# Kernel tuning notes

Hardware: AMD Instinct MI355X
Metric: run time of the kernel (lower is better)

Reference implementation:

```python
import math
import jax, jax.numpy as jnp
import numpy as np

B, S, HID, H = 2, 1024, 2048, 16
D = HID // H
HEAVY_RATIO = 0.1
RECENT_RATIO = 0.1
ROPE_BASE = 10000.0
N_KEEP_DIMS = 6  # eviction zeroes all but the 6 largest-|k| dims


def setup_inputs() -> dict:
    key = jax.random.key(0)
    k1, k2, k3, k4, k5 = jax.random.split(key, 5)
    std = 0.02
    hidden_states = jax.random.normal(k1, (B, S, HID), jnp.float32)
    wq = jax.random.normal(k2, (HID, HID), jnp.float32) * std
    wk = jax.random.normal(k3, (HID, HID), jnp.float32) * std
    wv = jax.random.normal(k4, (HID, HID), jnp.float32) * std
    wo = jax.random.normal(k5, (HID, HID), jnp.float32) * std
    neg = jnp.finfo(jnp.float32).min
    causal = jnp.tril(jnp.ones((S, S), bool))
    attention_mask = jnp.broadcast_to(
        jnp.where(causal, 0.0, neg)[None, None], (B, 1, S, S)
    ).astype(jnp.float32)
    return {"hidden_states": hidden_states, "wq": wq, "wk": wk, "wv": wv,
            "wo": wo, "attention_mask": attention_mask}


def _rotate_half(x):
    return jnp.concatenate([-x[..., D // 2:], x[..., :D // 2]], axis=-1)


def _apply_rope(q, k):
    inv_freq = 1.0 / (ROPE_BASE ** (jnp.arange(0, D, 2, dtype=jnp.float32) / D))
    t = jnp.arange(S, dtype=jnp.float32)
    freqs = jnp.outer(t, inv_freq)              # [S, D/2]
    emb = jnp.concatenate([freqs, freqs], -1)   # [S, D]
    cos = jnp.cos(emb)[None, None]              # [1,1,S,D]
    sin = jnp.sin(emb)[None, None]
    return q * cos + _rotate_half(q) * sin, k * cos + _rotate_half(k) * sin


def _h2o_attention(q, k, heavy_budget, recent_budget):
    """Faithful vectorized form of low_dimension_attention.

    The torch loop mutates key_states in place by zeroing the (D-6)
    smallest-magnitude dims of one evicted token per step. Since the
    small-dim set is fixed per (b,h) and zeroing is idempotent, we carry a
    boolean evicted mask instead of the mutated key tensor.
    """
    cache_budget = heavy_budget + recent_budget
    scale = 1.0 / math.sqrt(D)
    # small_dimensions: computed once at first trigger (t = cache_budget+1)
    # from the first cache_budget (unmutated) keys.
    mean_abs = jnp.abs(k[:, :, :cache_budget, :]).mean(axis=2)      # [B,H,D]
    ranks = jnp.argsort(jnp.argsort(mean_abs, axis=-1), axis=-1)
    small_mask = ranks < (D - N_KEEP_DIMS)                          # [B,H,D]
    sidx = jnp.arange(S)

    def step(carry, xs):
        hist, evicted, prev_attn = carry
        t, q_t = xs                                                 # q_t: [B,H,D]
        pred = t > cache_budget
        limit = t - recent_budget if recent_budget > 0 else t
        # eviction score = inf-mask history + previous step's raw scores
        scores = jnp.where(sidx < limit, hist + prev_attn, jnp.inf)  # [B,H,S]
        idx = jnp.argmin(scores, axis=-1)                            # [B,H]
        do = pred & (sidx[None, None, :] == idx[..., None])          # [B,H,S]
        evicted = evicted | do
        hist = jnp.where(do, jnp.inf, hist)
        k_eff = jnp.where(evicted[..., None] & small_mask[:, :, None, :], 0.0, k)
        attn = jnp.einsum('bhd,bhsd->bhs', q_t, k_eff) * scale
        attn = jnp.where(sidx <= t, attn, 0.0)
        return (hist, evicted, attn), attn

    init = (jnp.zeros((B, H, S), jnp.float32),
            jnp.zeros((B, H, S), bool),
            jnp.zeros((B, H, S), jnp.float32))
    q_seq = jnp.moveaxis(q, 2, 0)                                    # [S,B,H,D]
    _, rows = jax.lax.scan(step, init, (jnp.arange(S), q_seq))       # [S,B,H,S]
    return jnp.moveaxis(rows, 0, 2)                                  # [B,H,S,S]


def reference(hidden_states, wq, wk, wv, wo, attention_mask):
    heavy_budget = int(HEAVY_RATIO * S)
    recent_budget = int(RECENT_RATIO * S)
    q = (hidden_states @ wq).reshape(B, S, H, D).transpose(0, 2, 1, 3)
    k = (hidden_states @ wk).reshape(B, S, H, D).transpose(0, 2, 1, 3)
    v = (hidden_states @ wv).reshape(B, S, H, D).transpose(0, 2, 1, 3)
    q, k = _apply_rope(q, k)
    attn_weights = _h2o_attention(q, k, heavy_budget, recent_budget)  # [B,H,S,S]
    attn_weights = jnp.maximum(attn_weights + attention_mask,
                               jnp.finfo(jnp.float32).min)
    attn_weights = jax.nn.softmax(attn_weights, axis=-1)
    out = jnp.einsum('bhqk,bhkd->bhqd', attn_weights, v)
    out = out.transpose(0, 2, 1, 3).reshape(B, S, HID)
    return out @ wo
```

## Files before the change

### kernel.cpp

```cpp
#include <hip/hip_runtime.h>
#include <math.h>

#define S_LEN    1024
#define NHEAD    16
#define DHEAD    128
#define HIDDEN   2048
#define BATCH    2
#define BH       32
#define CACHE_B  204
#define RECENT_B 102
#define QK_SCALE 0.08838834764831845f

typedef float v2f __attribute__((ext_vector_type(2)));
typedef float f32x4 __attribute__((ext_vector_type(4)));
typedef short short8v __attribute__((ext_vector_type(8)));

__device__ __forceinline__ unsigned short f2bf(float f) {
  unsigned u = __float_as_uint(f);
  u += 0x7fffu + ((u >> 16) & 1u);
  return (unsigned short)(u >> 16);
}
__device__ __forceinline__ float bf2f(unsigned short h) {
  return __uint_as_float(((unsigned)h) << 16);
}

__device__ __forceinline__ void gl16(const void* g, void* l) {
  __builtin_amdgcn_global_load_lds(
      (const __attribute__((address_space(1))) unsigned int*)g,
      (__attribute__((address_space(3))) unsigned int*)l, 16, 0, 0);
}

__device__ __forceinline__ void mfma_b(f32x4& d, short8v a, short8v b) {
  asm("v_mfma_f32_16x16x32_bf16 %0, %1, %2, %0" : "+v"(d) : "v"(a), "v"(b));
}

__global__ __launch_bounds__(256) void split_a(
    const float* __restrict__ X, unsigned short* __restrict__ hi,
    unsigned short* __restrict__ lo) {
  const size_t i = ((size_t)blockIdx.x * 256 + threadIdx.x) * 4;
  const float4 v = *(const float4*)&X[i];
  const float f[4] = {v.x, v.y, v.z, v.w};
  unsigned short h[4], l[4];
#pragma unroll
  for (int j = 0; j < 4; ++j) {
    h[j] = f2bf(f[j]);
    l[j] = f2bf(f[j] - bf2f(h[j]));
  }
  *(ushort4*)&hi[i] = make_ushort4(h[0], h[1], h[2], h[3]);
  *(ushort4*)&lo[i] = make_ushort4(l[0], l[1], l[2], l[3]);
}

__global__ __launch_bounds__(256) void split_T(
    const float* __restrict__ W0, const float* __restrict__ W1,
    const float* __restrict__ W2, unsigned short* __restrict__ outB) {
  __shared__ float Ts[64][65];
  const float* W = (blockIdx.z == 0) ? W0 : ((blockIdx.z == 1) ? W1 : W2);
  unsigned short* hiT = outB + (size_t)blockIdx.z * 8388608u;
  unsigned short* loT = hiT + 4194304u;
  const int k0 = blockIdx.y * 64, n0 = blockIdx.x * 64;
  const int r = threadIdx.x >> 4, c4 = (threadIdx.x & 15) * 4;
#pragma unroll
  for (int it = 0; it < 4; ++it) {
    const float4 v =
        *(const float4*)&W[(size_t)(k0 + it * 16 + r) * HIDDEN + n0 + c4];
    Ts[it * 16 + r][c4 + 0] = v.x;
    Ts[it * 16 + r][c4 + 1] = v.y;
    Ts[it * 16 + r][c4 + 2] = v.z;
    Ts[it * 16 + r][c4 + 3] = v.w;
  }
  __syncthreads();
#pragma unroll
  for (int it = 0; it < 4; ++it) {
    const int n = it * 16 + r;
    unsigned short h[4], l[4];
#pragma unroll
    for (int j = 0; j < 4; ++j) {
      const float f = Ts[c4 + j][n];
      h[j] = f2bf(f);
      l[j] = f2bf(f - bf2f(h[j]));
    }
    const size_t o = (size_t)(n0 + n) * HIDDEN + k0 + c4;
    *(ushort4*)&hiT[o] = make_ushort4(h[0], h[1], h[2], h[3]);
    *(ushort4*)&loT[o] = make_ushort4(l[0], l[1], l[2], l[3]);
  }
}

template <int MODE>
__global__ __launch_bounds__(256) void gemm_mfma(
    const unsigned short* __restrict__ Ahi,
    const unsigned short* __restrict__ Alo,
    const unsigned short* __restrict__ WT, float* __restrict__ C0) {
  __shared__ unsigned short AhS[128][32];
  __shared__ unsigned short AlS[128][32];
  __shared__ unsigned short BhS[128][32];
  __shared__ unsigned short BlS[128][32];
  const int tid = threadIdx.x;
  const int lane = tid & 63;
  const int wv = tid >> 6;
  const int wr = wv >> 1, wc = wv & 1;
  const int m0 = blockIdx.y * 128, n0 = blockIdx.x * 128;
  const unsigned short* BhiT =
      WT + (MODE == 0 ? (size_t)blockIdx.z * 8388608u : (size_t)0);
  const unsigned short* BloT = BhiT + 4194304u;

  f32x4 acc[4][4];
#pragma unroll
  for (int i = 0; i < 4; ++i)
#pragma unroll
    for (int j = 0; j < 4; ++j) acc[i][j] = (f32x4)(0.0f);

  const int r_st = tid >> 2;
  const int kc_st = (tid & 3) * 8;

  for (int k0 = 0; k0 < HIDDEN; k0 += 32) {
#pragma unroll
    for (int l = 0; l < 2; ++l) {
      const int r = r_st + l * 64;
      const size_t ga = (size_t)(m0 + r) * HIDDEN + (k0 + kc_st);
      const size_t gb = (size_t)(n0 + r) * HIDDEN + (k0 + kc_st);
      gl16(Ahi + ga, &AhS[r][kc_st]);
      gl16(Alo + ga, &AlS[r][kc_st]);
      gl16(BhiT + gb, &BhS[r][kc_st]);
      gl16(BloT + gb, &BlS[r][kc_st]);
    }
    __syncthreads();
    const int mrow = lane & 15;
    const int kb = (lane >> 4) * 8;
    short8v ah[4], al[4], bh[4], bl[4];
#pragma unroll
    for (int i = 0; i < 4; ++i) {
      ah[i] = *(const short8v*)&AhS[wr * 64 + i * 16 + mrow][kb];
      al[i] = *(const short8v*)&AlS[wr * 64 + i * 16 + mrow][kb];
      bh[i] = *(const short8v*)&BhS[wc * 64 + i * 16 + mrow][kb];
      bl[i] = *(const short8v*)&BlS[wc * 64 + i * 16 + mrow][kb];
    }
#pragma unroll
    for (int i = 0; i < 4; ++i)
#pragma unroll
      for (int j = 0; j < 4; ++j) {
        mfma_b(acc[i][j], ah[i], bh[j]);
        mfma_b(acc[i][j], al[i], bh[j]);
        mfma_b(acc[i][j], ah[i], bl[j]);
      }
    __syncthreads();
  }

  float* C = C0;
  if (MODE == 0) C += (size_t)blockIdx.z * ((size_t)BH * S_LEN * DHEAD);
#pragma unroll
  for (int i = 0; i < 4; ++i) {
    const int mbase = m0 + wr * 64 + i * 16 + ((lane >> 4) * 4);
#pragma unroll
    for (int j = 0; j < 4; ++j) {
      const int n = n0 + wc * 64 + j * 16 + (lane & 15);
#pragma unroll
      for (int rg = 0; rg < 4; ++rg) {
        const int m = mbase + rg;
        const float val = acc[i][j][rg];
        if (MODE == 0) {
          const int b = m >> 10, s = m & (S_LEN - 1);
          const int h = n >> 7, d = n & (DHEAD - 1);
          C[(((size_t)(b * NHEAD + h) * S_LEN + s) * DHEAD) + d] = val;
        } else {
          C[(size_t)m * HIDDEN + n] = val;
        }
      }
    }
  }
}

__global__ __launch_bounds__(256) void rope_qk(float* __restrict__ Q,
                                               float* __restrict__ K) {
  int g = blockIdx.x * 4 + (threadIdx.x >> 6);
  int lane = threadIdx.x & 63;
  int s = g & (S_LEN - 1);
  double invf = exp(-((double)(2 * lane) / 128.0) * log(10000.0));
  float angle = (float)s * (float)invf;
  float c = (float)cos((double)angle);
  float sn = (float)sin((double)angle);
  size_t base = (size_t)g * DHEAD;
  float q0 = Q[base + lane], q1 = Q[base + lane + 64];
  Q[base + lane] = q0 * c - q1 * sn;
  Q[base + lane + 64] = q1 * c + q0 * sn;
  float k0 = K[base + lane], k1 = K[base + lane + 64];
  K[base + lane] = k0 * c - k1 * sn;
  K[base + lane + 64] = k1 * c + k0 * sn;
}

__global__ __launch_bounds__(128) void keep_pack(
    const float* __restrict__ Q, const float* __restrict__ K,
    float* __restrict__ Qp, float* __restrict__ Kp) {
  int bh = blockIdx.x;
  int d = threadIdx.x;
  __shared__ float ma[128];
  __shared__ int kf[128];
  __shared__ int kidx[8];
  const float* Kb = K + (size_t)bh * S_LEN * DHEAD;
  const float* Qb = Q + (size_t)bh * S_LEN * DHEAD;
  float sum = 0.0f;
  for (int s = 0; s < CACHE_B; ++s) sum += fabsf(Kb[(size_t)s * DHEAD + d]);
  ma[d] = sum / 204.0f;
  __syncthreads();
  float v = ma[d];
  int rank = 0;
  for (int e = 0; e < 128; ++e) {
    float u = ma[e];
    rank += (u < v) || (u == v && e < d);
  }
  int keep = (rank >= 128 - 6);
  kf[d] = keep;
  __syncthreads();
  if (keep) {
    int pos = 0;
    for (int e = 0; e < d; ++e) pos += kf[e];
    kidx[pos] = d;
  }
  __syncthreads();
  int i0 = kidx[0], i1 = kidx[1], i2 = kidx[2];
  int i3 = kidx[3], i4 = kidx[4], i5 = kidx[5];
  for (int s = threadIdx.x; s < S_LEN; s += 128) {
    size_t src = (size_t)s * DHEAD;
    size_t dst = ((size_t)bh * S_LEN + s) * 8;
    Qp[dst + 0] = Qb[src + i0]; Qp[dst + 1] = Qb[src + i1];
    Qp[dst + 2] = Qb[src + i2]; Qp[dst + 3] = Qb[src + i3];
    Qp[dst + 4] = Qb[src + i4]; Qp[dst + 5] = Qb[src + i5];
    Kp[dst + 0] = Kb[src + i0]; Kp[dst + 1] = Kb[src + i1];
    Kp[dst + 2] = Kb[src + i2]; Kp[dst + 3] = Kb[src + i3];
    Kp[dst + 4] = Kb[src + i4]; Kp[dst + 5] = Kb[src + i5];
  }
}

__global__ __launch_bounds__(256) void qkt_scores(
    const float* __restrict__ Q, const float* __restrict__ K,
    float* __restrict__ Af) {
  if (blockIdx.x > blockIdx.y) return;
  __shared__ float Qs[16][132];
  __shared__ float Ks[16][132];
  const int bh = blockIdx.z;
  const int tid = threadIdx.x;
  const int tx = tid & 15, ty = tid >> 4;
  const int m0 = blockIdx.y * 128, n0 = blockIdx.x * 128;
  const float* Qb = Q + (size_t)bh * S_LEN * DHEAD;
  const float* Kb = K + (size_t)bh * S_LEN * DHEAD;
  v2f acc[8][4];
#pragma unroll
  for (int i = 0; i < 8; ++i)
#pragma unroll
    for (int p = 0; p < 4; ++p) acc[i][p] = (v2f)(0.0f);

  for (int k0 = 0; k0 < DHEAD; k0 += 16) {
#pragma unroll
    for (int l = 0; l < 2; ++l) {
      int f = tid + l * 256;
      int r = f >> 2, c = (f & 3) * 4;
      const float4 q = *(const float4*)&Qb[(size_t)(m0 + r) * DHEAD + k0 + c];
      Qs[c + 0][r] = q.x; Qs[c + 1][r] = q.y;
      Qs[c + 2][r] = q.z; Qs[c + 3][r] = q.w;
      const float4 kv = *(const float4*)&Kb[(size_t)(n0 + r) * DHEAD + k0 + c];
      Ks[c + 0][r] = kv.x; Ks[c + 1][r] = kv.y;
      Ks[c + 2][r] = kv.z; Ks[c + 3][r] = kv.w;
    }
    __syncthreads();
#pragma unroll
    for (int kk = 0; kk < 16; ++kk) {
      float av[8];
      v2f bv[4];
      *(float4*)&av[0] = *(float4*)&Qs[kk][ty * 4];
      *(float4*)&av[4] = *(float4*)&Qs[kk][64 + ty * 4];
      const float4 b0 = *(const float4*)&Ks[kk][tx * 4];
      const float4 b1 = *(const float4*)&Ks[kk][64 + tx * 4];
      bv[0] = (v2f){b0.x, b0.y};
      bv[1] = (v2f){b0.z, b0.w};
      bv[2] = (v2f){b1.x, b1.y};
      bv[3] = (v2f){b1.z, b1.w};
#pragma unroll
      for (int i = 0; i < 8; ++i) {
        const v2f a2 = (v2f){av[i], av[i]};
#pragma unroll
        for (int p = 0; p < 4; ++p) acc[i][p] = a2 * bv[p] + acc[i][p];
      }
    }
    __syncthreads();
  }
  float* Cb = Af + (size_t)bh * S_LEN * S_LEN;
#pragma unroll
  for (int gi = 0; gi < 2; ++gi)
#pragma unroll
    for (int i = 0; i < 4; ++i) {
      const int t = m0 + gi * 64 + ty * 4 + i;
      const int ia = gi * 4 + i;
#pragma unroll
      for (int gj = 0; gj < 2; ++gj) {
        const int s = n0 + gj * 64 + tx * 4;
        float4 o;
        o.x = acc[ia][gj * 2 + 0].x * QK_SCALE;
        o.y = acc[ia][gj * 2 + 0].y * QK_SCALE;
        o.z = acc[ia][gj * 2 + 1].x * QK_SCALE;
        o.w = acc[ia][gj * 2 + 1].y * QK_SCALE;
        *(float4*)&Cb[(size_t)t * S_LEN + s] = o;
      }
    }
}

template <int CTRL, int RMASK>
__device__ __forceinline__ float dpp_fmin(float x) {
  const int xi = __builtin_bit_cast(int, x);
  const int y = __builtin_amdgcn_update_dpp(xi, xi, CTRL, RMASK, 0xF, false);
  return fminf(x, __builtin_bit_cast(float, y));
}
__device__ __forceinline__ float wave_min_f32(float x) {
  x = dpp_fmin<0x111, 0xF>(x);
  x = dpp_fmin<0x112, 0xF>(x);
  x = dpp_fmin<0x114, 0xF>(x);
  x = dpp_fmin<0x118, 0xF>(x);
  x = dpp_fmin<0x142, 0xA>(x);
  x = dpp_fmin<0x143, 0xC>(x);
  return __builtin_bit_cast(
      float, __builtin_amdgcn_readlane(__builtin_bit_cast(int, x), 63));
}

__global__ __launch_bounds__(64, 1) void scan_evict(
    const float* __restrict__ Af, int* __restrict__ evt) {
  __shared__ int evt_lds[S_LEN];
  const int bh = blockIdx.x;
  const int lane = threadIdx.x;
  const float* Ab = Af + (size_t)bh * S_LEN * S_LEN;
  int* evtb = evt + bh * S_LEN;

  {
    const int4 big = make_int4(0x7fffffff, 0x7fffffff, 0x7fffffff, 0x7fffffff);
#pragma unroll
    for (int j = 0; j < 4; ++j) *(int4*)&evt_lds[j * 256 + lane * 4] = big;
  }

  unsigned evmask = 0;
  unsigned elig = (lane < 6) ? 0xFFFFu : (lane == 6 ? 0x7Fu : 0u);

  const float* lb = Ab + lane * 16;
  float4 A0[4], A1[4], A2[4], A3[4], A4[4], A5[4];

#define SB() __builtin_amdgcn_sched_barrier(0)

#define LDROW(R, r)                                      \
  do {                                                   \
    int r_ = (r);                                        \
    r_ = r_ > 1022 ? 1022 : r_;                          \
    const float* rb = lb + (size_t)r_ * S_LEN;           \
    R[0] = *(const float4*)(rb + 0);                     \
    R[1] = *(const float4*)(rb + 4);                     \
    R[2] = *(const float4*)(rb + 8);                     \
    R[3] = *(const float4*)(rb + 12);                    \
  } while (0)

#define STEP(R, T)                                                          \
  do {                                                                      \
    const int t_ = (T);                                                     \
    const int snew = t_ - 103;      \
    elig |= ((snew >> 4) == lane) ? (1u << (snew & 15)) : 0u;               \
    const unsigned ue = elig & ~evmask;                                     \
    float fv[16];                                                           \
    _Pragma("unroll") for (int p = 0; p < 4; ++p) {                         \
      fv[p * 4 + 0] = ((ue >> (p * 4 + 0)) & 1u) ? R[p].x : INFINITY;       \
      fv[p * 4 + 1] = ((ue >> (p * 4 + 1)) & 1u) ? R[p].y : INFINITY;       \
      fv[p * 4 + 2] = ((ue >> (p * 4 + 2)) & 1u) ? R[p].z : INFINITY;       \
      fv[p * 4 + 3] = ((ue >> (p * 4 + 3)) & 1u) ? R[p].w : INFINITY;       \
    }                                                                       \
            \
    float m8[8]; int s8[8];                                                 \
    _Pragma("unroll") for (int i = 0; i < 8; ++i) {                         \
      m8[i] = fminf(fv[2 * i], fv[2 * i + 1]);                              \
      s8[i] = (fv[2 * i] <= fv[2 * i + 1]) ? (2 * i) : (2 * i + 1);         \
    }                                                                       \
    float m4[4]; int s4[4];                                                 \
    _Pragma("unroll") for (int i = 0; i < 4; ++i) {                         \
      m4[i] = fminf(m8[2 * i], m8[2 * i + 1]);                              \
      s4[i] = (m8[2 * i] <= m8[2 * i + 1]) ? s8[2 * i] : s8[2 * i + 1];     \
    }                                                                       \
    float m2[2]; int s2[2];                                                 \
    m2[0] = fminf(m4[0], m4[1]); s2[0] = (m4[0] <= m4[1]) ? s4[0] : s4[1];  \
    m2[1] = fminf(m4[2], m4[3]); s2[1] = (m4[2] <= m4[3]) ? s4[2] : s4[3];  \
    const float vmin = fminf(m2[0], m2[1]);                                 \
    const int bloc = (m2[0] <= m2[1]) ? s2[0] : s2[1];                      \
    const float best = wave_min_f32(vmin);                                  \
    const unsigned long long msk = __ballot(vmin == best);                  \
    const int winner = __ffsll(msk) - 1;        \
    if (lane == winner) {                                                   \
      evmask |= 1u << bloc;                                                 \
      evt_lds[lane * 16 + bloc] = t_;     \
    }                                                                       \
  } while (0)

  LDROW(A0, 204); LDROW(A1, 205); LDROW(A2, 206);
  LDROW(A3, 207); LDROW(A4, 208); LDROW(A5, 209);
  SB();

  for (int g = 0; g < 136; ++g) {
    const int t0 = 205 + g * 6;
    STEP(A0, t0 + 0); LDROW(A0, t0 + 5); SB();
    STEP(A1, t0 + 1); LDROW(A1, t0 + 6); SB();
    STEP(A2, t0 + 2); LDROW(A2, t0 + 7); SB();
    STEP(A3, t0 + 3); LDROW(A3, t0 + 8); SB();
    STEP(A4, t0 + 4); LDROW(A4, t0 + 9); SB();
    STEP(A5, t0 + 5); LDROW(A5, t0 + 10); SB();
  }
  STEP(A0, 1021);
  STEP(A1, 1022);
  STEP(A2, 1023);

  asm volatile("s_waitcnt lgkmcnt(0)" ::: "memory");
  SB();
#pragma unroll
  for (int j = 0; j < 4; ++j)
    *(int4*)&evtb[j * 256 + lane * 4] =
        *(const int4*)&evt_lds[j * 256 + lane * 4];
#undef LDROW
#undef STEP
#undef SB
}

__global__ __launch_bounds__(256) void attn_av(
    const float* __restrict__ Af, const float* __restrict__ Qp,
    const float* __restrict__ Kp, const int* __restrict__ evt,
    const float* __restrict__ V, float* __restrict__ AO) {
  const int t0 = blockIdx.x * 8;
  const int bh = blockIdx.y;
  __shared__ float P[8][S_LEN];
  __shared__ float rinv[8];
  const int tid = threadIdx.x;
  const int lane = tid & 63, wave = tid >> 6;
  const float* Ab = Af + (size_t)bh * S_LEN * S_LEN;
  const int* eb = evt + bh * S_LEN;
  const float* Kpb = Kp + (size_t)bh * S_LEN * 8;

  for (int rr = 0; rr < 2; ++rr) {
    const int r = wave * 2 + rr;
    const int t = t0 + r;
    float qp[6];
#pragma unroll
    for (int j = 0; j < 6; ++j) qp[j] = Qp[((size_t)bh * S_LEN + t) * 8 + j];
    float vals[16];
    float m = -INFINITY;
#pragma unroll
    for (int i = 0; i < 16; ++i) {
      int s = lane + i * 64;
      float sc = 0.0f;
      if (s <= t) {
        if (eb[s] <= t) {
          const float* kr = &Kpb[(size_t)s * 8];
          sc = QK_SCALE * (qp[0] * kr[0] + qp[1] * kr[1] + qp[2] * kr[2] +
                           qp[3] * kr[3] + qp[4] * kr[4] + qp[5] * kr[5]);
        } else {
          sc = Ab[(size_t)t * S_LEN + s];
        }
        m = fmaxf(m, sc);
      }
      vals[i] = sc;
    }
    for (int off = 32; off; off >>= 1) m = fmaxf(m, __shfl_xor(m, off, 64));
    float sum = 0.0f;
#pragma unroll
    for (int i = 0; i < 16; ++i) {
      int s = lane + i * 64;
      float p = 0.0f;
      if (s <= t) {
        p = expf(vals[i] - m);
        sum += p;
      }
      P[r][s] = p;
    }
    for (int off = 32; off; off >>= 1) sum += __shfl_xor(sum, off, 64);
    if (lane == 0) rinv[r] = 1.0f / sum;
  }
  __syncthreads();

  const int d4 = (tid & 31) * 4;
  const int r = tid >> 5;
  const int t = t0 + r;
  const float* Vb = V + (size_t)bh * S_LEN * DHEAD;
  float ax = 0.f, ay = 0.f, az = 0.f, aw = 0.f;
  const int smax = t0 + 7;
  for (int s4 = 0; s4 <= smax; s4 += 4) {
    const float4 p4 = *(const float4*)&P[r][s4];
    const float4 v0 = *(const float4*)&Vb[(size_t)(s4 + 0) * DHEAD + d4];
    const float4 v1 = *(const float4*)&Vb[(size_t)(s4 + 1) * DHEAD + d4];
    const float4 v2 = *(const float4*)&Vb[(size_t)(s4 + 2) * DHEAD + d4];
    const float4 v3 = *(const float4*)&Vb[(size_t)(s4 + 3) * DHEAD + d4];
    ax += p4.x * v0.x + p4.y * v1.x + p4.z * v2.x + p4.w * v3.x;
    ay += p4.x * v0.y + p4.y * v1.y + p4.z * v2.y + p4.w * v3.y;
    az += p4.x * v0.z + p4.y * v1.z + p4.z * v2.z + p4.w * v3.z;
    aw += p4.x * v0.w + p4.y * v1.w + p4.z * v2.w + p4.w * v3.w;
  }
  const float ri = rinv[r];
  const int b = bh >> 4, h = bh & 15;
  float4 o;
  o.x = ax * ri; o.y = ay * ri; o.z = az * ri; o.w = aw * ri;
  *(float4*)&AO[((size_t)(b * S_LEN + t)) * HIDDEN + h * DHEAD + d4] = o;
}

extern "C" void kernel_launch(void* const* d_in, const int* in_sizes, int n_in,
                              void* d_out, int out_size, void* d_ws,
                              size_t ws_size, hipStream_t stream) {
  const float* hs = (const float*)d_in[0];
  const float* wq = (const float*)d_in[1];
  const float* wk = (const float*)d_in[2];
  const float* wv = (const float*)d_in[3];
  const float* wo = (const float*)d_in[4];
  float* out = (float*)d_out;

  const size_t SZ_QKV = (size_t)BH * S_LEN * DHEAD;
  float* Q = (float*)d_ws;
  float* K = Q + SZ_QKV;
  float* V = K + SZ_QKV;
  float* Af = V + SZ_QKV;
  float* Qp = Af + (size_t)BH * S_LEN * S_LEN;
  float* Kp = Qp + (size_t)BH * S_LEN * 8;
  int* evt = (int*)(Kp + (size_t)BH * S_LEN * 8);
  float* AO = (float*)(evt + BH * S_LEN);

  unsigned short* U = (unsigned short*)Af;
  unsigned short* wT = U;
  unsigned short* hs_hi = U + 25165824u;
  unsigned short* hs_lo = hs_hi + 4194304u;
  unsigned short* ao_hi = U;
  unsigned short* ao_lo = U + 4194304u;
  unsigned short* woT = U + 8388608u;

  split_T<<<dim3(32, 32, 3), 256, 0, stream>>>(wq, wk, wv, wT);
  split_a<<<dim3(4096), 256, 0, stream>>>(hs, hs_hi, hs_lo);
  gemm_mfma<0><<<dim3(16, 16, 3), 256, 0, stream>>>(hs_hi, hs_lo, wT, Q);
  rope_qk<<<dim3(BH * S_LEN / 4), 256, 0, stream>>>(Q, K);
  keep_pack<<<dim3(BH), 128, 0, stream>>>(Q, K, Qp, Kp);
  qkt_scores<<<dim3(8, 8, BH), 256, 0, stream>>>(Q, K, Af);
  scan_evict<<<dim3(BH), 64, 0, stream>>>(Af, evt);
  attn_av<<<dim3(S_LEN / 8, BH), 256, 0, stream>>>(Af, Qp, Kp, evt, V, AO);
  split_a<<<dim3(4096), 256, 0, stream>>>(AO, ao_hi, ao_lo);
  split_T<<<dim3(32, 32, 1), 256, 0, stream>>>(wo, wo, wo, woT);
  gemm_mfma<1><<<dim3(16, 16, 1), 256, 0, stream>>>(ao_hi, ao_lo, woT, out);
}
```

Before: 1.220 ms.

## Transpose packed keys and split attention-V across waves with V reuse

The packed low-dimension keys are now stored dimension-major, so lanes read consecutive addresses instead of strided 8-float rows. The score loop becomes branch-free: it always loads both the full score and the low-rank dot product and selects between them. The P·V stage is restructured so each wave handles a strided subset of key chunks for all 8 rows, reusing each V load across 8 rows, and the partial sums are then reduced through shared memory. The cost is extra unconditional loads of masked scores, and extra shared-memory reduction and synchronisation.

```diff
diff --git a/kernel.cpp b/kernel.cpp
--- a/kernel.cpp
+++ b/kernel.cpp
@@ -189,7 +189,7 @@
 
 __global__ __launch_bounds__(128) void keep_pack(
     const float* __restrict__ Q, const float* __restrict__ K,
-    float* __restrict__ Qp, float* __restrict__ Kp) {
+    float* __restrict__ Qp, float* __restrict__ KpT) {
   int bh = blockIdx.x;
   int d = threadIdx.x;
   __shared__ float ma[128];
@@ -218,15 +218,19 @@
   __syncthreads();
   int i0 = kidx[0], i1 = kidx[1], i2 = kidx[2];
   int i3 = kidx[3], i4 = kidx[4], i5 = kidx[5];
+  float* Kt = KpT + (size_t)bh * 6 * S_LEN;
   for (int s = threadIdx.x; s < S_LEN; s += 128) {
     size_t src = (size_t)s * DHEAD;
     size_t dst = ((size_t)bh * S_LEN + s) * 8;
     Qp[dst + 0] = Qb[src + i0]; Qp[dst + 1] = Qb[src + i1];
     Qp[dst + 2] = Qb[src + i2]; Qp[dst + 3] = Qb[src + i3];
     Qp[dst + 4] = Qb[src + i4]; Qp[dst + 5] = Qb[src + i5];
-    Kp[dst + 0] = Kb[src + i0]; Kp[dst + 1] = Kb[src + i1];
-    Kp[dst + 2] = Kb[src + i2]; Kp[dst + 3] = Kb[src + i3];
-    Kp[dst + 4] = Kb[src + i4]; Kp[dst + 5] = Kb[src + i5];
+    Kt[0 * S_LEN + s] = Kb[src + i0];
+    Kt[1 * S_LEN + s] = Kb[src + i1];
+    Kt[2 * S_LEN + s] = Kb[src + i2];
+    Kt[3 * S_LEN + s] = Kb[src + i3];
+    Kt[4 * S_LEN + s] = Kb[src + i4];
+    Kt[5 * S_LEN + s] = Kb[src + i5];
   }
 }
 
@@ -420,7 +424,7 @@
 
 __global__ __launch_bounds__(256) void attn_av(
     const float* __restrict__ Af, const float* __restrict__ Qp,
-    const float* __restrict__ Kp, const int* __restrict__ evt,
+    const float* __restrict__ KpT, const int* __restrict__ evt,
     const float* __restrict__ V, float* __restrict__ AO) {
   const int t0 = blockIdx.x * 8;
   const int bh = blockIdx.y;
@@ -430,7 +434,7 @@
   const int lane = tid & 63, wave = tid >> 6;
   const float* Ab = Af + (size_t)bh * S_LEN * S_LEN;
   const int* eb = evt + bh * S_LEN;
-  const float* Kpb = Kp + (size_t)bh * S_LEN * 8;
+  const float* Kt = KpT + (size_t)bh * 6 * S_LEN;
 
   for (int rr = 0; rr < 2; ++rr) {
     const int r = wave * 2 + rr;
@@ -442,30 +446,27 @@
     float m = -INFINITY;
 #pragma unroll
     for (int i = 0; i < 16; ++i) {
-      int s = lane + i * 64;
-      float sc = 0.0f;
-      if (s <= t) {
-        if (eb[s] <= t) {
-          const float* kr = &Kpb[(size_t)s * 8];
-          sc = QK_SCALE * (qp[0] * kr[0] + qp[1] * kr[1] + qp[2] * kr[2] +
-                           qp[3] * kr[3] + qp[4] * kr[4] + qp[5] * kr[5]);
-        } else {
-          sc = Ab[(size_t)t * S_LEN + s];
-        }
-        m = fmaxf(m, sc);
-      }
+      const int s = lane + i * 64;
+      const float full = Ab[(size_t)t * S_LEN + s];
+      float low = qp[0] * Kt[s];
+      low += qp[1] * Kt[S_LEN + s];
+      low += qp[2] * Kt[2 * S_LEN + s];
+      low += qp[3] * Kt[3 * S_LEN + s];
+      low += qp[4] * Kt[4 * S_LEN + s];
+      low += qp[5] * Kt[5 * S_LEN + s];
+      const int ev = eb[s];
+      const float sc = (ev <= t) ? (QK_SCALE * low) : full;
       vals[i] = sc;
+      m = fmaxf(m, (s <= t) ? sc : -INFINITY);
     }
     for (int off = 32; off; off >>= 1) m = fmaxf(m, __shfl_xor(m, off, 64));
     float sum = 0.0f;
 #pragma unroll
     for (int i = 0; i < 16; ++i) {
-      int s = lane + i * 64;
-      float p = 0.0f;
-      if (s <= t) {
-        p = expf(vals[i] - m);
-        sum += p;
-      }
+      const int s = lane + i * 64;
+      const float e = expf(vals[i] - m);
+      const float p = (s <= t) ? e : 0.0f;
+      sum += p;
       P[r][s] = p;
     }
     for (int off = 32; off; off >>= 1) sum += __shfl_xor(sum, off, 64);
@@ -473,27 +474,49 @@
   }
   __syncthreads();
 
+  const int NC = (t0 + 8) >> 2;
+  const float* Vb = V + (size_t)bh * S_LEN * DHEAD;
+  const int d2 = lane * 2;
+  float accx[8], accy[8];
+#pragma unroll
+  for (int r = 0; r < 8; ++r) { accx[r] = 0.0f; accy[r] = 0.0f; }
+  for (int c = wave; c < NC; c += 4) {
+    const int s0 = c * 4;
+    float4 p4[8];
+#pragma unroll
+    for (int r = 0; r < 8; ++r) p4[r] = *(const float4*)&P[r][s0];
+    const float2 v0 = *(const float2*)&Vb[(size_t)(s0 + 0) * DHEAD + d2];
+    const float2 v1 = *(const float2*)&Vb[(size_t)(s0 + 1) * DHEAD + d2];
+    const float2 v2 = *(const float2*)&Vb[(size_t)(s0 + 2) * DHEAD + d2];
+    const float2 v3 = *(const float2*)&Vb[(size_t)(s0 + 3) * DHEAD + d2];
+#pragma unroll
+    for (int r = 0; r < 8; ++r) {
+      accx[r] += p4[r].x * v0.x + p4[r].y * v1.x + p4[r].z * v2.x +
+                 p4[r].w * v3.x;
+      accy[r] += p4[r].x * v0.y + p4[r].y * v1.y + p4[r].z * v2.y +
+                 p4[r].w * v3.y;
+    }
+  }
+  __syncthreads();
+  float* red = &P[0][0];
+#pragma unroll
+  for (int r = 0; r < 8; ++r) {
+    float2 pr; pr.x = accx[r]; pr.y = accy[r];
+    *(float2*)&red[((wave * 8 + r) << 7) + d2] = pr;
+  }
+  __syncthreads();
+  const int r = tid >> 5;
   const int d4 = (tid & 31) * 4;
-  const int r = tid >> 5;
   const int t = t0 + r;
-  const float* Vb = V + (size_t)bh * S_LEN * DHEAD;
-  float ax = 0.f, ay = 0.f, az = 0.f, aw = 0.f;
-  const int smax = t0 + 7;
-  for (int s4 = 0; s4 <= smax; s4 += 4) {
-    const float4 p4 = *(const float4*)&P[r][s4];
-    const float4 v0 = *(const float4*)&Vb[(size_t)(s4 + 0) * DHEAD + d4];
-    const float4 v1 = *(const float4*)&Vb[(size_t)(s4 + 1) * DHEAD + d4];
-    const float4 v2 = *(const float4*)&Vb[(size_t)(s4 + 2) * DHEAD + d4];
-    const float4 v3 = *(const float4*)&Vb[(size_t)(s4 + 3) * DHEAD + d4];
-    ax += p4.x * v0.x + p4.y * v1.x + p4.z * v2.x + p4.w * v3.x;
-    ay += p4.x * v0.y + p4.y * v1.y + p4.z * v2.y + p4.w * v3.y;
-    az += p4.x * v0.z + p4.y * v1.z + p4.z * v2.z + p4.w * v3.z;
-    aw += p4.x * v0.w + p4.y * v1.w + p4.z * v2.w + p4.w * v3.w;
+  float4 o = make_float4(0.f, 0.f, 0.f, 0.f);
+#pragma unroll
+  for (int w = 0; w < 4; ++w) {
+    const float4 part = *(const float4*)&red[((w * 8 + r) << 7) + d4];
+    o.x += part.x; o.y += part.y; o.z += part.z; o.w += part.w;
   }
   const float ri = rinv[r];
+  o.x *= ri; o.y *= ri; o.z *= ri; o.w *= ri;
   const int b = bh >> 4, h = bh & 15;
-  float4 o;
-  o.x = ax * ri; o.y = ay * ri; o.z = az * ri; o.w = aw * ri;
   *(float4*)&AO[((size_t)(b * S_LEN + t)) * HIDDEN + h * DHEAD + d4] = o;
 }
 
@@ -513,8 +536,8 @@
   float* V = K + SZ_QKV;
   float* Af = V + SZ_QKV;
   float* Qp = Af + (size_t)BH * S_LEN * S_LEN;
-  float* Kp = Qp + (size_t)BH * S_LEN * 8;
-  int* evt = (int*)(Kp + (size_t)BH * S_LEN * 8);
+  float* KpT = Qp + (size_t)BH * S_LEN * 8;
+  int* evt = (int*)(KpT + (size_t)BH * S_LEN * 8);
   float* AO = (float*)(evt + BH * S_LEN);
 
   unsigned short* U = (unsigned short*)Af;
@@ -529,10 +552,10 @@
   split_a<<<dim3(4096), 256, 0, stream>>>(hs, hs_hi, hs_lo);
   gemm_mfma<0><<<dim3(16, 16, 3), 256, 0, stream>>>(hs_hi, hs_lo, wT, Q);
   rope_qk<<<dim3(BH * S_LEN / 4), 256, 0, stream>>>(Q, K);
-  keep_pack<<<dim3(BH), 128, 0, stream>>>(Q, K, Qp, Kp);
+  keep_pack<<<dim3(BH), 128, 0, stream>>>(Q, K, Qp, KpT);
   qkt_scores<<<dim3(8, 8, BH), 256, 0, stream>>>(Q, K, Af);
   scan_evict<<<dim3(BH), 64, 0, stream>>>(Af, evt);
-  attn_av<<<dim3(S_LEN / 8, BH), 256, 0, stream>>>(Af, Qp, Kp, evt, V, AO);
+  attn_av<<<dim3(S_LEN / 8, BH), 256, 0, stream>>>(Af, Qp, KpT, evt, V, AO);
   split_a<<<dim3(4096), 256, 0, stream>>>(AO, ao_hi, ao_lo);
   split_T<<<dim3(32, 32, 1), 256, 0, stream>>>(wo, wo, wo, woT);
   gemm_mfma<1><<<dim3(16, 16, 1), 256, 0, stream>>>(ao_hi, ao_lo, woT, out);
```

Result: faster. 1.002 ms (-17.9%).
